# Optimization experiments

Measured on AMD Instinct MI355X. Metric: run time of the kernel, lower is better.

Reference implementation:

```python
import jax, jax.numpy as jnp
import numpy as np

E = 1024      # embedding_size
H = 16        # num_head
DQ = DK = DV = 64  # per-head q/k/v size


def setup_inputs() -> dict:
    key = jax.random.key(0)
    ks = jax.random.split(key, 9)
    B, S = 2, 2048
    s = 1.0 / np.sqrt(E)
    return {
        "q": jax.random.normal(ks[0], (B, S, E), jnp.float32),
        "k": jax.random.normal(ks[1], (B, S, E), jnp.float32),
        "v": jax.random.normal(ks[2], (B, S, E), jnp.float32),
        "w_q": jax.random.normal(ks[3], (E, H * DQ), jnp.float32) * s,
        "b_q": jax.random.normal(ks[4], (H * DQ,), jnp.float32) * s,
        "w_k": jax.random.normal(ks[5], (E, H * DK), jnp.float32) * s,
        "b_k": jax.random.normal(ks[6], (H * DK,), jnp.float32) * s,
        "w_v": jax.random.normal(ks[7], (E, H * DV), jnp.float32) * s,
        "b_v": jax.random.normal(ks[8], (H * DV,), jnp.float32) * s,
    }


def reference(q, k, v, w_q, b_q, w_k, b_k, w_v, b_v):
    B, Sq, _ = q.shape
    Sk = k.shape[1]
    # projections -> [B, S, H, d] -> [B, H, S, d]
    qh = (q @ w_q + b_q).reshape(B, Sq, H, DQ).transpose(0, 2, 1, 3)
    kh = (k @ w_k + b_k).reshape(B, Sk, H, DK).transpose(0, 2, 1, 3)
    vh = (v @ w_v + b_v).reshape(B, Sk, H, DV).transpose(0, 2, 1, 3)
    # scaled dot-product attention; scores [B, H, Sq, Sk]
    scores = jnp.einsum("bhqd,bhkd->bhqk", qh, kh) / jnp.sqrt(jnp.float32(DQ))
    weights = jax.nn.softmax(scores, axis=-1)
    out = jnp.einsum("bhqk,bhkd->bhqd", weights, vh)  # [B, H, Sq, DV]
    return out.transpose(0, 2, 1, 3).reshape(B, Sq, H * DV)
```

## Files before the change

kernel.cpp:

```cpp
#include <hip/hip_runtime.h>
#include <hip/hip_bf16.h>

typedef __bf16 bf16_t;
typedef bf16_t bf16x8 __attribute__((ext_vector_type(8)));
typedef bf16_t bf16x4 __attribute__((ext_vector_type(4)));
typedef short  short4v __attribute__((ext_vector_type(4)));
typedef float  f32x4  __attribute__((ext_vector_type(4)));

#define MFMA16(a,b,c) __builtin_amdgcn_mfma_f32_16x16x32_bf16(a, b, c, 0, 0, 0)

constexpr int S = 2048, H = 16, Dh = 64;
constexpr int N = H * Dh;
constexpr int K = 1024;
constexpr float QSCALE = 0.125f * 1.4426950408889634f;

static __device__ inline void load_lds16(const bf16_t* g, bf16_t* l) {
  __builtin_amdgcn_global_load_lds(
      (const __attribute__((address_space(1))) void*)g,
      (__attribute__((address_space(3))) void*)l, 16, 0, 0);
}

static __device__ inline ushort f2bb(float x) {
  bf16_t h = (bf16_t)x;
  return __builtin_bit_cast(ushort, h);
}

__global__ __launch_bounds__(256) void prep(
    const float* __restrict__ q, const float* __restrict__ k,
    const float* __restrict__ v,
    const float* __restrict__ wq, const float* __restrict__ wk,
    const float* __restrict__ wv,
    bf16_t* __restrict__ xq, bf16_t* __restrict__ xk, bf16_t* __restrict__ xv,
    bf16_t* __restrict__ wtq, bf16_t* __restrict__ wtk, bf16_t* __restrict__ wtv) {
  __shared__ ushort tile[64][68];
  int bx = blockIdx.x, t = threadIdx.x;
  if (bx < 6144) {
    int z = bx >> 11, bb = bx & 2047;
    const float* xi = z == 0 ? q : z == 1 ? k : v;
    bf16_t*      xo = z == 0 ? xq : z == 1 ? xk : xv;
    size_t idx = ((size_t)bb * 256 + t) * 8;
    float4 a = *(const float4*)&xi[idx];
    float4 b = *(const float4*)&xi[idx + 4];
    bf16x8 w;
    w[0] = (bf16_t)a.x; w[1] = (bf16_t)a.y; w[2] = (bf16_t)a.z; w[3] = (bf16_t)a.w;
    w[4] = (bf16_t)b.x; w[5] = (bf16_t)b.y; w[6] = (bf16_t)b.z; w[7] = (bf16_t)b.w;
    *(bf16x8*)&xo[idx] = w;
  } else {
    int zz = bx - 6144;
    int z = zz >> 8, bb = zz & 255;
    const float* wi = z == 0 ? wq : z == 1 ? wk : wv;
    ushort*      wo = (ushort*)(z == 0 ? wtq : z == 1 ? wtk : wtv);
    int k0 = (bb >> 4) * 64, n0 = (bb & 15) * 64;
    for (int i = 0; i < 4; ++i) {
      int idx4 = (i * 256 + t) * 4;
      int r = idx4 >> 6, c = idx4 & 63;
      float4 vv = *(const float4*)&wi[(size_t)(k0 + r) * N + n0 + c];
      tile[r][c] = f2bb(vv.x); tile[r][c + 1] = f2bb(vv.y);
      tile[r][c + 2] = f2bb(vv.z); tile[r][c + 3] = f2bb(vv.w);
    }
    __syncthreads();
    for (int i = 0; i < 4; ++i) {
      int idx4 = (i * 256 + t) * 4;
      int r = idx4 >> 6, c = idx4 & 63;
      ushort4 vv;
      vv.x = tile[c][r]; vv.y = tile[c + 1][r];
      vv.z = tile[c + 2][r]; vv.w = tile[c + 3][r];
      *(ushort4*)&wo[(size_t)(n0 + r) * K + k0 + c] = vv;
    }
  }
}

__global__ __launch_bounds__(256) void proj_gemm(
    const bf16_t* __restrict__ xq, const bf16_t* __restrict__ xk,
    const bf16_t* __restrict__ xv,
    const bf16_t* __restrict__ wtq, const bf16_t* __restrict__ wtk,
    const bf16_t* __restrict__ wtv,
    const float* __restrict__ bq, const float* __restrict__ bk,
    const float* __restrict__ bv,
    bf16_t* __restrict__ qh, bf16_t* __restrict__ kh, bf16_t* __restrict__ vt) {
  int mode = blockIdx.z;
  const bf16_t* X  = mode == 0 ? xq  : mode == 1 ? xk  : wtv;
  const bf16_t* Wt = mode == 0 ? wtq : mode == 1 ? wtk : xv;
  const float*  Bi = mode == 0 ? bq  : mode == 1 ? bk  : bv;

  __shared__ __align__(16) bf16_t smem[17408];
  bf16_t (*Ash)[64] = (bf16_t(*)[64])smem;
  bf16_t (*Bsh)[64] = (bf16_t(*)[64])(smem + 8192);
  bf16_t* Cs = smem;

  int tid = threadIdx.x;
  int wave = tid >> 6, lane = tid & 63;
  int lr = lane & 15, lg = lane >> 4;
  int lrow = lane >> 3, lchunk = lane & 7;
  int m0 = (mode < 2 ? blockIdx.y : blockIdx.x) * 128;
  int n0 = (mode < 2 ? blockIdx.x : blockIdx.y) * 128;
  int wm = (wave >> 1) * 64, wn = (wave & 1) * 64;

  f32x4 acc[4][4];
  for (int i = 0; i < 4; ++i)
    for (int j = 0; j < 4; ++j) acc[i][j] = (f32x4){0.f, 0.f, 0.f, 0.f};

  for (int ko = 0; ko < K / 64; ++ko) {
    __syncthreads();
    for (int j = 0; j < 4; ++j) {
      int r = wave * 32 + j * 8 + lrow;
      int gc = (lchunk ^ (r & 7)) * 8;
      load_lds16(&X [(size_t)(m0 + r) * K + ko * 64 + gc], &Ash[r][lchunk * 8]);
      load_lds16(&Wt[(size_t)(n0 + r) * K + ko * 64 + gc], &Bsh[r][lchunk * 8]);
    }
    __syncthreads();
    for (int kk = 0; kk < 2; ++kk) {
      bf16x8 af[4], bfr[4];
      for (int i = 0; i < 4; ++i) {
        int rr = wm + i * 16 + lr;
        af[i] = *(const bf16x8*)&Ash[rr][(((kk << 2) | lg) ^ (rr & 7)) * 8];
      }
      for (int j = 0; j < 4; ++j) {
        int rr = wn + j * 16 + lr;
        bfr[j] = *(const bf16x8*)&Bsh[rr][(((kk << 2) | lg) ^ (rr & 7)) * 8];
      }
      for (int i = 0; i < 4; ++i)
        for (int j = 0; j < 4; ++j)
          acc[i][j] = MFMA16(af[i], bfr[j], acc[i][j]);
    }
  }

  float badd[4][4][4];
  if (mode < 2) {
    float bvv[4];
    for (int j = 0; j < 4; ++j) bvv[j] = Bi[n0 + wn + j * 16 + lr];
    for (int i = 0; i < 4; ++i)
      for (int j = 0; j < 4; ++j)
        for (int r = 0; r < 4; ++r) badd[i][j][r] = bvv[j];
  } else {
    for (int i = 0; i < 4; ++i)
      for (int r = 0; r < 4; ++r) {
        float bm = Bi[m0 + wm + i * 16 + lg * 4 + r];
        for (int j = 0; j < 4; ++j) badd[i][j][r] = bm;
      }
  }

  __syncthreads();
  for (int i = 0; i < 4; ++i)
    for (int j = 0; j < 4; ++j)
      for (int r = 0; r < 4; ++r) {
        float vvv = acc[i][j][r] + badd[i][j][r];
        if (mode == 0) vvv *= QSCALE;
        Cs[(size_t)(wm + i * 16 + lg * 4 + r) * 136 + wn + j * 16 + lr] = (bf16_t)vvv;
      }
  __syncthreads();

  bf16_t* o = mode == 0 ? qh : mode == 1 ? kh : vt;
  for (int p = 0; p < 8; ++p) {
    int idx = p * 256 + tid;
    int row = idx >> 4, ch = idx & 15;
    bf16x8 vv = *(const bf16x8*)&Cs[(size_t)row * 136 + ch * 8];
    size_t dst;
    if (mode < 2) {
      int m_g = m0 + row, n_g = n0 + ch * 8;
      int b = m_g >> 11, s = m_g & 2047;
      int h = n_g >> 6, d = n_g & 63;
      dst = (((size_t)(b * 16 + h) * 2048) + s) * 64 + d;
    } else {
      int w_g = m0 + row, t_g = n0 + ch * 8;
      int b = t_g >> 11, s = t_g & 2047;
      dst = ((size_t)(b * 1024 + w_g)) * 2048 + s;
    }
    *(uint4*)&o[dst] = __builtin_bit_cast(uint4, vv);
  }
}

__global__ __launch_bounds__(512) void attn(
    const bf16_t* __restrict__ qh, const bf16_t* __restrict__ kh,
    const bf16_t* __restrict__ vt, float* __restrict__ out) {
  __shared__ __align__(16) bf16_t smem[8192];
  bf16_t* kt = smem;
  bf16_t* vs = smem + 4096;

  int tid = threadIdx.x, wave = tid >> 6, lane = tid & 63;
  int lr = lane & 15, lg = lane >> 4;
  int bh = blockIdx.y;
  int q0 = blockIdx.x * 128 + wave * 16;

  const bf16_t* qg = qh + (size_t)bh * S * Dh;
  const bf16_t* kg = kh + (size_t)bh * S * Dh;
  const bf16_t* vg = vt + (size_t)bh * Dh * S;

  bf16x8 bqf[2];
  for (int kk = 0; kk < 2; ++kk)
    bqf[kk] = *(const bf16x8*)&qg[(size_t)(q0 + lr) * 64 + kk * 32 + lg * 8];

  bf16x8 ones8;
  for (int j = 0; j < 8; ++j) ones8[j] = (bf16_t)1.0f;

  f32x4 o_acc[4], lacc;
  lacc = (f32x4){0.f, 0.f, 0.f, 0.f};
  for (int dt = 0; dt < 4; ++dt) o_acc[dt] = (f32x4){0.f, 0.f, 0.f, 0.f};

  int srow = tid >> 3, schunk = tid & 7;
  int sgc = (schunk ^ (srow & 7)) * 8;
  int ld = srow * 64 + schunk * 8;

  uint4 kr = *(const uint4*)&kg[(size_t)srow * 64 + sgc];
  uint4 vr = *(const uint4*)&vg[(size_t)srow * S + sgc];

  int sw = lr & 7, p4 = (lg & 1) * 4;

  constexpr int NIT = S / 64;
  for (int it = 0; it < NIT; ++it) {
    __syncthreads();
    *(uint4*)&kt[ld] = kr;
    *(uint4*)&vs[ld] = vr;
    if (it + 1 < NIT) {
      int sk1 = (it + 1) * 64;
      kr = *(const uint4*)&kg[(size_t)(sk1 + srow) * 64 + sgc];
      vr = *(const uint4*)&vg[(size_t)srow * S + sk1 + sgc];
    }
    __syncthreads();

    bf16x8 ak[4][2];
    for (int t = 0; t < 4; ++t)
      for (int kk = 0; kk < 2; ++kk)
        ak[t][kk] = *(const bf16x8*)
            &kt[(t * 16 + lr) * 64 + ((kk * 4 + lg) ^ sw) * 8];

    f32x4 st[4];
    for (int t = 0; t < 4; ++t) st[t] = (f32x4){0.f, 0.f, 0.f, 0.f};
    for (int kk = 0; kk < 2; ++kk)
      for (int t = 0; t < 4; ++t)
        st[t] = MFMA16(ak[t][kk], bqf[kk], st[t]);

    bf16x8 pa8[2];
    for (int tp = 0; tp < 2; ++tp)
      for (int r = 0; r < 4; ++r) {
        pa8[tp][r]     = (bf16_t)__builtin_amdgcn_exp2f(st[2 * tp][r]);
        pa8[tp][r + 4] = (bf16_t)__builtin_amdgcn_exp2f(st[2 * tp + 1][r]);
      }

    for (int tp = 0; tp < 2; ++tp) {
      int g0 = tp * 4 + (lg >> 1);
      bf16x8 bb[4];
      for (int dt = 0; dt < 4; ++dt) {
        const bf16_t* vrow = &vs[(dt * 16 + lr) * 64];
        bf16x4 lo = *(const bf16x4*)&vrow[((g0      ^ sw) * 8) + p4];
        bf16x4 hi = *(const bf16x4*)&vrow[(((g0 + 2) ^ sw) * 8) + p4];
        for (int j = 0; j < 4; ++j) { bb[dt][j] = lo[j]; bb[dt][j + 4] = hi[j]; }
      }
      for (int dt = 0; dt < 4; ++dt)
        o_acc[dt] = MFMA16(pa8[tp], bb[dt], o_acc[dt]);
      lacc = MFMA16(pa8[tp], ones8, lacc);
    }
  }

  int b = bh >> 4, h = bh & 15;
  for (int r = 0; r < 4; ++r) {
    float inv = 1.f / lacc[r];
    int s_row = q0 + lg * 4 + r;
    size_t base = ((size_t)(b * S + s_row)) * 1024 + h * 64;
    for (int dt = 0; dt < 4; ++dt)
      out[base + dt * 16 + lr] = o_acc[dt][r] * inv;
  }
}

extern "C" void kernel_launch(void* const* d_in, const int* in_sizes, int n_in,
                              void* d_out, int out_size, void* d_ws, size_t ws_size,
                              hipStream_t stream) {
  const float* q  = (const float*)d_in[0];
  const float* k  = (const float*)d_in[1];
  const float* v  = (const float*)d_in[2];
  const float* wq = (const float*)d_in[3];
  const float* bq = (const float*)d_in[4];
  const float* wk = (const float*)d_in[5];
  const float* bk = (const float*)d_in[6];
  const float* wv = (const float*)d_in[7];
  const float* bv = (const float*)d_in[8];

  bf16_t* ws  = (bf16_t*)d_ws;
  constexpr size_t MW = (size_t)1 << 20;
  constexpr size_t MX = (size_t)4096 * 1024;
  bf16_t* wtq = ws;
  bf16_t* wtk = wtq + MW;
  bf16_t* wtv = wtk + MW;
  bf16_t* xq  = wtv + MW;
  bf16_t* xk  = xq + MX;
  bf16_t* xv  = xk + MX;
  bf16_t* qhd = xv + MX;
  bf16_t* khd = qhd + MX;
  bf16_t* vtd = khd + MX;
  float* out  = (float*)d_out;

  prep<<<6912, 256, 0, stream>>>(q, k, v, wq, wk, wv,
                                 xq, xk, xv, wtq, wtk, wtv);
  proj_gemm<<<dim3(8, 32, 3), 256, 0, stream>>>(xq, xk, xv, wtq, wtk, wtv,
                                                bq, bk, bv, qhd, khd, vtd);
  attn<<<dim3(16, 32), 512, 0, stream>>>(qhd, khd, vtd, out);
}
```

Baseline: 203.4 us.

## Split attention KV range across two wave groups and double query rows per wave

The attention kernel now splits its 8 waves into two halves, and each half processes a separate half of the key/value sequence in its own shared-memory buffer. Each wave handles 32 query rows instead of 16, so every K tile loaded from LDS is reused for two query subtiles. At the end, the second half writes its partial numerators and row sums to shared memory, and the first half combines them and normalizes. The point is better K/V fragment reuse and a shorter serial loop per block, paid for with more registers, twice the LDS, and an extra reduction step.

```diff
diff --git a/kernel.cpp b/kernel.cpp
--- a/kernel.cpp
+++ b/kernel.cpp
@@ -170,95 +170,158 @@
   }
 }
 
-__global__ __launch_bounds__(512) void attn(
+__global__ __launch_bounds__(512, 4) void attn(
     const bf16_t* __restrict__ qh, const bf16_t* __restrict__ kh,
     const bf16_t* __restrict__ vt, float* __restrict__ out) {
-  __shared__ __align__(16) bf16_t smem[8192];
-  bf16_t* kt = smem;
-  bf16_t* vs = smem + 4096;
+  __shared__ __align__(16) bf16_t smem[16640];
 
   int tid = threadIdx.x, wave = tid >> 6, lane = tid & 63;
   int lr = lane & 15, lg = lane >> 4;
+  int half = wave >> 2, w4 = wave & 3;
   int bh = blockIdx.y;
-  int q0 = blockIdx.x * 128 + wave * 16;
+  int q0 = blockIdx.x * 128 + w4 * 32;
+
+  bf16_t* kt = smem + half * 8192;
+  bf16_t* vs = kt + 4096;
 
   const bf16_t* qg = qh + (size_t)bh * S * Dh;
   const bf16_t* kg = kh + (size_t)bh * S * Dh;
   const bf16_t* vg = vt + (size_t)bh * Dh * S;
 
-  bf16x8 bqf[2];
-  for (int kk = 0; kk < 2; ++kk)
-    bqf[kk] = *(const bf16x8*)&qg[(size_t)(q0 + lr) * 64 + kk * 32 + lg * 8];
+  bf16x8 bqf[2][2];
+#pragma unroll
+  for (int ms = 0; ms < 2; ++ms)
+#pragma unroll
+    for (int kk = 0; kk < 2; ++kk)
+      bqf[ms][kk] = *(const bf16x8*)
+          &qg[(size_t)(q0 + ms * 16 + lr) * 64 + kk * 32 + lg * 8];
 
   bf16x8 ones8;
+#pragma unroll
   for (int j = 0; j < 8; ++j) ones8[j] = (bf16_t)1.0f;
 
-  f32x4 o_acc[4], lacc;
-  lacc = (f32x4){0.f, 0.f, 0.f, 0.f};
-  for (int dt = 0; dt < 4; ++dt) o_acc[dt] = (f32x4){0.f, 0.f, 0.f, 0.f};
-
-  int srow = tid >> 3, schunk = tid & 7;
-  int sgc = (schunk ^ (srow & 7)) * 8;
-  int ld = srow * 64 + schunk * 8;
-
-  uint4 kr = *(const uint4*)&kg[(size_t)srow * 64 + sgc];
-  uint4 vr = *(const uint4*)&vg[(size_t)srow * S + sgc];
+  f32x4 o_acc[2][4], lacc[2];
+#pragma unroll
+  for (int ms = 0; ms < 2; ++ms) {
+    lacc[ms] = (f32x4){0.f, 0.f, 0.f, 0.f};
+#pragma unroll
+    for (int dt = 0; dt < 4; ++dt) o_acc[ms][dt] = (f32x4){0.f, 0.f, 0.f, 0.f};
+  }
+
+  int lrow = lane >> 3, lchunk = lane & 7;
+  int srow0 = w4 * 16 + lrow;
+  int srow1 = srow0 + 8;
+  int sgc = (lchunk ^ (srow0 & 7)) * 8;
+  int ld0 = srow0 * 64 + lchunk * 8;
+  int ld1 = srow1 * 64 + lchunk * 8;
+
+  int cb = half * (S / 2);
+
+  uint4 kr0 = *(const uint4*)&kg[(size_t)(cb + srow0) * 64 + sgc];
+  uint4 kr1 = *(const uint4*)&kg[(size_t)(cb + srow1) * 64 + sgc];
+  uint4 vr0 = *(const uint4*)&vg[(size_t)srow0 * S + cb + sgc];
+  uint4 vr1 = *(const uint4*)&vg[(size_t)srow1 * S + cb + sgc];
 
   int sw = lr & 7, p4 = (lg & 1) * 4;
 
-  constexpr int NIT = S / 64;
-  for (int it = 0; it < NIT; ++it) {
-    __syncthreads();
-    *(uint4*)&kt[ld] = kr;
-    *(uint4*)&vs[ld] = vr;
-    if (it + 1 < NIT) {
-      int sk1 = (it + 1) * 64;
-      kr = *(const uint4*)&kg[(size_t)(sk1 + srow) * 64 + sgc];
-      vr = *(const uint4*)&vg[(size_t)srow * S + sk1 + sgc];
+  constexpr int NITH = (S / 2) / 64;
+  for (int it = 0; it < NITH; ++it) {
+    __syncthreads();
+    *(uint4*)&kt[ld0] = kr0;
+    *(uint4*)&kt[ld1] = kr1;
+    *(uint4*)&vs[ld0] = vr0;
+    *(uint4*)&vs[ld1] = vr1;
+    if (it + 1 < NITH) {
+      int sk1 = cb + (it + 1) * 64;
+      kr0 = *(const uint4*)&kg[(size_t)(sk1 + srow0) * 64 + sgc];
+      kr1 = *(const uint4*)&kg[(size_t)(sk1 + srow1) * 64 + sgc];
+      vr0 = *(const uint4*)&vg[(size_t)srow0 * S + sk1 + sgc];
+      vr1 = *(const uint4*)&vg[(size_t)srow1 * S + sk1 + sgc];
     }
     __syncthreads();
 
     bf16x8 ak[4][2];
+#pragma unroll
     for (int t = 0; t < 4; ++t)
+#pragma unroll
       for (int kk = 0; kk < 2; ++kk)
         ak[t][kk] = *(const bf16x8*)
             &kt[(t * 16 + lr) * 64 + ((kk * 4 + lg) ^ sw) * 8];
 
-    f32x4 st[4];
-    for (int t = 0; t < 4; ++t) st[t] = (f32x4){0.f, 0.f, 0.f, 0.f};
-    for (int kk = 0; kk < 2; ++kk)
-      for (int t = 0; t < 4; ++t)
-        st[t] = MFMA16(ak[t][kk], bqf[kk], st[t]);
-
-    bf16x8 pa8[2];
-    for (int tp = 0; tp < 2; ++tp)
-      for (int r = 0; r < 4; ++r) {
-        pa8[tp][r]     = (bf16_t)__builtin_amdgcn_exp2f(st[2 * tp][r]);
-        pa8[tp][r + 4] = (bf16_t)__builtin_amdgcn_exp2f(st[2 * tp + 1][r]);
-      }
-
+    bf16x8 pa8[2][2];
+#pragma unroll
+    for (int ms = 0; ms < 2; ++ms) {
+      f32x4 st[4];
+#pragma unroll
+      for (int t = 0; t < 4; ++t) st[t] = (f32x4){0.f, 0.f, 0.f, 0.f};
+#pragma unroll
+      for (int kk = 0; kk < 2; ++kk)
+#pragma unroll
+        for (int t = 0; t < 4; ++t)
+          st[t] = MFMA16(ak[t][kk], bqf[ms][kk], st[t]);
+#pragma unroll
+      for (int tp = 0; tp < 2; ++tp)
+#pragma unroll
+        for (int r = 0; r < 4; ++r) {
+          pa8[ms][tp][r]     = (bf16_t)__builtin_amdgcn_exp2f(st[2 * tp][r]);
+          pa8[ms][tp][r + 4] = (bf16_t)__builtin_amdgcn_exp2f(st[2 * tp + 1][r]);
+        }
+    }
+
+#pragma unroll
     for (int tp = 0; tp < 2; ++tp) {
       int g0 = tp * 4 + (lg >> 1);
       bf16x8 bb[4];
+#pragma unroll
       for (int dt = 0; dt < 4; ++dt) {
         const bf16_t* vrow = &vs[(dt * 16 + lr) * 64];
         bf16x4 lo = *(const bf16x4*)&vrow[((g0      ^ sw) * 8) + p4];
         bf16x4 hi = *(const bf16x4*)&vrow[(((g0 + 2) ^ sw) * 8) + p4];
+#pragma unroll
         for (int j = 0; j < 4; ++j) { bb[dt][j] = lo[j]; bb[dt][j + 4] = hi[j]; }
       }
-      for (int dt = 0; dt < 4; ++dt)
-        o_acc[dt] = MFMA16(pa8[tp], bb[dt], o_acc[dt]);
-      lacc = MFMA16(pa8[tp], ones8, lacc);
-    }
-  }
-
-  int b = bh >> 4, h = bh & 15;
-  for (int r = 0; r < 4; ++r) {
-    float inv = 1.f / lacc[r];
-    int s_row = q0 + lg * 4 + r;
-    size_t base = ((size_t)(b * S + s_row)) * 1024 + h * 64;
-    for (int dt = 0; dt < 4; ++dt)
-      out[base + dt * 16 + lr] = o_acc[dt][r] * inv;
+#pragma unroll
+      for (int ms = 0; ms < 2; ++ms) {
+#pragma unroll
+        for (int dt = 0; dt < 4; ++dt)
+          o_acc[ms][dt] = MFMA16(pa8[ms][tp], bb[dt], o_acc[ms][dt]);
+        lacc[ms] = MFMA16(pa8[ms][tp], ones8, lacc[ms]);
+      }
+    }
+  }
+
+  __syncthreads();
+  float* mo = (float*)smem;
+  float* ls = mo + 8 * 16 * 64;
+
+  if (half == 1) {
+#pragma unroll
+    for (int ms = 0; ms < 2; ++ms)
+#pragma unroll
+      for (int r = 0; r < 4; ++r) {
+        int row = (w4 * 2 + ms) * 16 + lg * 4 + r;
+#pragma unroll
+        for (int dt = 0; dt < 4; ++dt)
+          mo[row * 64 + dt * 16 + lr] = o_acc[ms][dt][r];
+        if (lr == 0) ls[row] = lacc[ms][r];
+      }
+  }
+  __syncthreads();
+  if (half == 0) {
+    int b = bh >> 4, hh = bh & 15;
+#pragma unroll
+    for (int ms = 0; ms < 2; ++ms)
+#pragma unroll
+      for (int r = 0; r < 4; ++r) {
+        int row = (w4 * 2 + ms) * 16 + lg * 4 + r;
+        float inv = 1.f / (lacc[ms][r] + ls[row]);
+        int s_row = q0 + ms * 16 + lg * 4 + r;
+        size_t base = ((size_t)(b * S + s_row)) * 1024 + hh * 64;
+#pragma unroll
+        for (int dt = 0; dt < 4; ++dt)
+          out[base + dt * 16 + lr] =
+              (o_acc[ms][dt][r] + mo[row * 64 + dt * 16 + lr]) * inv;
+      }
   }
 }
 
```

Result: slower. 243.0 us (+19.5%).
